# Kernel optimization log

Measured on AMD Instinct MI355X. Metric: run time of the kernel, lower is better.

The kernel has to match this reference:

```python
import jax, jax.numpy as jnp
import numpy as np

TOPK = 2
ROUTE_SCALE = 1.0


def setup_inputs() -> dict:
    key = jax.random.key(0)
    ks = jax.random.split(key, 9)
    B, T, C, E, H = 4, 2048, 1024, 8, 2752
    s = 0.02  # init scale for weights
    return {
        "x": jax.random.normal(ks[0], (B, T, C), dtype=jnp.float32),
        "gate_w": jax.random.normal(ks[1], (E, C), dtype=jnp.float32) * s,
        "expert_bias": jnp.zeros((E,), dtype=jnp.float32),
        "w1": jax.random.normal(ks[2], (E, C, H), dtype=jnp.float32) * s,
        "w2": jax.random.normal(ks[3], (E, H, C), dtype=jnp.float32) * s,
        "w3": jax.random.normal(ks[4], (E, C, H), dtype=jnp.float32) * s,
        "sw1": jax.random.normal(ks[5], (C, H), dtype=jnp.float32) * s,
        "sw2": jax.random.normal(ks[6], (H, C), dtype=jnp.float32) * s,
        "sw3": jax.random.normal(ks[7], (C, H), dtype=jnp.float32) * s,
    }


def reference(x, gate_w, expert_bias, w1, w2, w3, sw1, sw2, sw3):
    B, T, C = x.shape
    E = gate_w.shape[0]
    xf = x.reshape(-1, C)  # (N, C)
    N = xf.shape[0]

    # --- ExpertGate (sigmoid scoring, aux-loss-free, eval mode) ---
    scores = jax.nn.sigmoid(xf @ gate_w.T)            # (N, E), original scores
    routing = scores + expert_bias[None, :]           # bias only affects selection
    _, idx = jax.lax.top_k(routing, TOPK)             # (N, TOPK)
    w = jnp.take_along_axis(scores, idx, axis=1)      # gather original scores
    w = w / (w.sum(axis=-1, keepdims=True) + 1e-8)    # sigmoid normalization
    w = w * ROUTE_SCALE

    # Scatter top-k weights into a dense (N, E) combine matrix
    gates = jnp.zeros((N, E), dtype=xf.dtype)
    gates = gates.at[jnp.arange(N)[:, None], idx].add(w)

    # --- Routed SwiGLU experts (dense compute, gated combine) ---
    y = jnp.zeros_like(xf)
    for e in range(E):  # small fixed loop over experts
        h = jax.nn.silu(xf @ w1[e]) * (xf @ w3[e])    # (N, H)
        y = y + gates[:, e:e + 1] * (h @ w2[e])

    # --- Shared expert (always on) ---
    y = y + (jax.nn.silu(xf @ sw1) * (xf @ sw3)) @ sw2

    return y.reshape(B, T, C)
```

## Files before the change

### kernel.cpp

```cpp
#include <hip/hip_runtime.h>
#include <hip/hip_bf16.h>
#include <stdint.h>

#define E_ 8
#define C_ 1024
#define H_ 2752
#define NTOK 8192
#define CAP_ROWS 17408
#define ROUTED_XB 136
#define SHARED_XB 64
#define SHARED_HBASE 17408
#define HROWS 25600

typedef unsigned short u16;
typedef __attribute__((ext_vector_type(8))) short bf16x8;
typedef __attribute__((ext_vector_type(4))) float f32x4;

static constexpr size_t SZ_XB    = (size_t)NTOK * C_ * 2;
static constexpr size_t SZ_WT    = (size_t)E_ * H_ * C_ * 2;
static constexpr size_t SZ_SWT   = (size_t)H_ * C_ * 2;
static constexpr size_t SZ_H     = (size_t)HROWS * H_ * 2;

static constexpr size_t OFF_XB   = 0;
static constexpr size_t OFF_W1T  = OFF_XB   + SZ_XB;
static constexpr size_t OFF_W3T  = OFF_W1T  + SZ_WT;
static constexpr size_t OFF_W2T  = OFF_W3T  + SZ_WT;
static constexpr size_t OFF_SW1T = OFF_W2T  + SZ_WT;
static constexpr size_t OFF_SW3T = OFF_SW1T + SZ_SWT;
static constexpr size_t OFF_SW2T = OFF_SW3T + SZ_SWT;
static constexpr size_t OFF_H    = OFF_SW2T + SZ_SWT;
static constexpr size_t OFF_RIDX = OFF_H    + SZ_H;
static constexpr size_t OFF_RW   = OFF_RIDX + (size_t)NTOK*2*4;
static constexpr size_t OFF_OFFS = OFF_RW   + (size_t)NTOK*2*4;
static constexpr size_t OFF_PTOK = OFF_OFFS + 64;
static constexpr size_t OFF_PW   = OFF_PTOK + (size_t)CAP_ROWS*4;
static constexpr size_t OFF_INV  = OFF_PW   + (size_t)CAP_ROWS*4;
static constexpr size_t WS_NEED  = OFF_INV  + (size_t)NTOK*2*4;

static constexpr size_t OFF_OUT  = OFF_W1T;

__device__ __forceinline__ u16 f2bf(float f) {
  union { float f; uint32_t u; } v; v.f = f;
  uint32_t r = v.u + 0x7FFFu + ((v.u >> 16) & 1u);
  return (u16)(r >> 16);
}
__device__ __forceinline__ float bfu(uint32_t v) {
  union { uint32_t u; float f; } x; x.u = v << 16; return x.f;
}

__device__ __forceinline__ void gld16(const void* g, void* l) {
  uint32_t lo = (uint32_t)(uintptr_t)l;
  lo = __builtin_amdgcn_readfirstlane(lo);
  __builtin_amdgcn_global_load_lds(
      (const __attribute__((address_space(1))) void*)g,
      (__attribute__((address_space(3))) void*)(uintptr_t)lo, 16, 0, 0);
}

#define MFMA16(A,B,C) __builtin_amdgcn_mfma_f32_16x16x32_bf16((A),(B),(C),0,0,0)

__global__ __launch_bounds__(256) void gate_kernel(
    const float* __restrict__ x, const float* __restrict__ gw,
    const float* __restrict__ bias, u16* __restrict__ xb,
    int* __restrict__ ridx, float* __restrict__ rw)
{
  const int n = blockIdx.x, t = threadIdx.x;
  const float4 v = *(const float4*)(x + (size_t)n * C_ + t * 4);
  union { u16 u[4]; uint2 d; } pk;
  pk.u[0] = f2bf(v.x); pk.u[1] = f2bf(v.y); pk.u[2] = f2bf(v.z); pk.u[3] = f2bf(v.w);
  *(uint2*)(xb + (size_t)n * C_ + t * 4) = pk.d;

  float p[E_];
#pragma unroll
  for (int e = 0; e < E_; ++e) {
    const float4 g = *(const float4*)(gw + (size_t)e * C_ + t * 4);
    p[e] = v.x * g.x + v.y * g.y + v.z * g.z + v.w * g.w;
  }
#pragma unroll
  for (int e = 0; e < E_; ++e)
    for (int off = 32; off > 0; off >>= 1) p[e] += __shfl_down(p[e], off);

  __shared__ float red[4][E_];
  const int wv = t >> 6;
  if ((t & 63) == 0) {
#pragma unroll
    for (int e = 0; e < E_; ++e) red[wv][e] = p[e];
  }
  __syncthreads();
  if (t == 0) {
    float sc[E_], rt[E_];
#pragma unroll
    for (int e = 0; e < E_; ++e) {
      const float d = red[0][e] + red[1][e] + red[2][e] + red[3][e];
      const float s = 1.f / (1.f + expf(-d));
      sc[e] = s; rt[e] = s + bias[e];
    }
    int i0 = 0; float b0 = rt[0];
#pragma unroll
    for (int e = 1; e < E_; ++e) if (rt[e] > b0) { b0 = rt[e]; i0 = e; }
    int i1 = -1; float b1 = -1e30f;
#pragma unroll
    for (int e = 0; e < E_; ++e) if (e != i0 && rt[e] > b1) { b1 = rt[e]; i1 = e; }
    const float s0 = sc[i0], s1 = sc[i1];
    const float inv = 1.f / (s0 + s1 + 1e-8f);
    ridx[2 * n] = i0; ridx[2 * n + 1] = i1;
    rw[2 * n] = s0 * inv; rw[2 * n + 1] = s1 * inv;
  }
}

__global__ __launch_bounds__(256) void transpose_cs_kernel(
    const float* __restrict__ w1, const float* __restrict__ w3,
    const float* __restrict__ sw1, const float* __restrict__ sw3,
    u16* __restrict__ w1t, u16* __restrict__ w3t,
    u16* __restrict__ sw1t, u16* __restrict__ sw3t)
{
  const int z = blockIdx.z;
  const float* src; u16* dst;
  if      (z < 8)  { src = w1 + (size_t)z * C_ * H_;       dst = w1t + (size_t)z * H_ * C_; }
  else if (z < 16) { src = w3 + (size_t)(z - 8) * C_ * H_; dst = w3t + (size_t)(z - 8) * H_ * C_; }
  else if (z == 16){ src = sw1; dst = sw1t; }
  else             { src = sw3; dst = sw3t; }
  __shared__ float tile[32][33];
  const int tx = threadIdx.x, ty = threadIdx.y;
  const int s0 = blockIdx.x * 32;
  const int r0 = blockIdx.y * 32;
#pragma unroll
  for (int i = 0; i < 4; ++i)
    tile[ty + 8 * i][tx] = src[(size_t)(r0 + ty + 8 * i) * H_ + s0 + tx];
  __syncthreads();
#pragma unroll
  for (int i = 0; i < 4; ++i)
    dst[(size_t)(s0 + ty + 8 * i) * C_ + r0 + tx] = f2bf(tile[tx][ty + 8 * i]);
}

__global__ __launch_bounds__(256) void transpose_sc_kernel(
    const float* __restrict__ w2, const float* __restrict__ sw2,
    u16* __restrict__ w2t, u16* __restrict__ sw2t)
{
  const int z = blockIdx.z;
  const float* src; u16* dst;
  if (z < 8) { src = w2 + (size_t)z * H_ * C_; dst = w2t + (size_t)z * C_ * H_; }
  else       { src = sw2; dst = sw2t; }
  __shared__ float tile[32][33];
  const int tx = threadIdx.x, ty = threadIdx.y;
  const int s0 = blockIdx.x * 32;
  const int r0 = blockIdx.y * 32;
#pragma unroll
  for (int i = 0; i < 4; ++i)
    tile[ty + 8 * i][tx] = src[(size_t)(r0 + ty + 8 * i) * C_ + s0 + tx];
  __syncthreads();
#pragma unroll
  for (int i = 0; i < 4; ++i)
    dst[(size_t)(s0 + ty + 8 * i) * H_ + r0 + tx] = f2bf(tile[tx][ty + 8 * i]);
}

__global__ __launch_bounds__(256) void route_scan_kernel(
    const int* __restrict__ ridx, const float* __restrict__ rw,
    int* __restrict__ offsets, int* __restrict__ perm_tok,
    float* __restrict__ perm_w, int* __restrict__ invp)
{
  __shared__ int cnt[256][E_];
  __shared__ int pref[E_][257];
  __shared__ int offs[E_ + 1];
  __shared__ int totals[E_];
  const int t = threadIdx.x;
#pragma unroll
  for (int e = 0; e < E_; ++e) cnt[t][e] = 0;
  for (int j = 0; j < 64; ++j) { const int e = ridx[t * 64 + j]; cnt[t][e]++; }
  __syncthreads();
  if (t < E_) {
    int run = 0;
    for (int i = 0; i < 256; ++i) { pref[t][i] = run; run += cnt[i][t]; }
    totals[t] = run; pref[t][256] = run;
  }
  __syncthreads();
  if (t == 0) {
    int o = 0;
    for (int e = 0; e < E_; ++e) { offs[e] = o; o += (totals[e] + 127) & ~127; }
    offs[E_] = o;
    for (int i = 0; i <= E_; ++i) offsets[i] = offs[i];
  }
  __syncthreads();
#pragma unroll
  for (int e = 0; e < E_; ++e) cnt[t][e] = offs[e] + pref[e][t];
  for (int j = 0; j < 64; ++j) {
    const int a = t * 64 + j;
    const int e = ridx[a];
    const int p = cnt[t][e]++;
    perm_tok[p] = a >> 1;
    perm_w[p] = rw[a];
    invp[a] = p;
  }
  __syncthreads();
  for (int e = 0; e < E_; ++e) {
    for (int p = offs[e] + totals[e] + t; p < offs[e + 1]; p += 256) {
      perm_tok[p] = 0; perm_w[p] = 0.f;
    }
  }
}

__global__ __launch_bounds__(256, 2) void gemm1_m(
    const u16* __restrict__ xb, const u16* __restrict__ w1t_all,
    const u16* __restrict__ w3t_all, const u16* __restrict__ sw1t,
    const u16* __restrict__ sw3t, u16* __restrict__ hbuf,
    const int* __restrict__ offsets, const int* __restrict__ ptok)
{
  __shared__ u16 lds[3 * 8192];
  const int t = threadIdx.x;
  const int n0 = blockIdx.x * 128;
  const int by = blockIdx.y;

  const u16 *b1w, *b3w; int row0; size_t hr0; int gather;
  if (by < ROUTED_XB) {
    row0 = by * 128;
    if (row0 >= offsets[8]) return;
    int e = 0;
#pragma unroll
    for (int i = 0; i < 7; ++i) if (row0 >= offsets[i + 1]) e = i + 1;
    b1w = w1t_all + (size_t)e * (H_ * C_);
    b3w = w3t_all + (size_t)e * (H_ * C_);
    hr0 = (size_t)row0; gather = 1;
  } else {
    row0 = (by - ROUTED_XB) * 128;
    b1w = sw1t; b3w = sw3t; hr0 = (size_t)SHARED_HBASE + row0; gather = 0;
  }

  const int tq = t >> 3;
  const int cb = (((t & 7) ^ (tq & 7)) << 4);
  const char* gA[4]; const char* gB1[4]; const char* gB3[4];
#pragma unroll
  for (int i = 0; i < 4; ++i) {
    const int m = i * 32 + tq;
    const int tok = gather ? ptok[row0 + m] : (row0 + m);
    gA[i] = (const char*)xb + (size_t)tok * (C_ * 2) + cb;
    int nn = n0 + m; if (nn > H_ - 1) nn = H_ - 1;
    gB1[i] = (const char*)b1w + (size_t)nn * (C_ * 2) + cb;
    gB3[i] = (const char*)b3w + (size_t)nn * (C_ * 2) + cb;
  }
  char* lwave = (char*)lds + (t >> 6) * 1024;

  f32x4 acc1[4][4], acc3[4][4];
#pragma unroll
  for (int i = 0; i < 4; ++i)
#pragma unroll
    for (int j = 0; j < 4; ++j) { acc1[i][j] = f32x4{0,0,0,0}; acc3[i][j] = f32x4{0,0,0,0}; }

  const int lane = t & 63;
  const int l15 = lane & 15, lhi = lane >> 4, swz = lane & 7;
  const int wm = (t >> 7) & 1, wn = (t >> 6) & 1;
  int arow[4], brow[4];
#pragma unroll
  for (int f = 0; f < 4; ++f) {
    arow[f] = (wm * 64 + f * 16 + l15) * 128;
    brow[f] = (wn * 64 + f * 16 + l15) * 128;
  }
  const char* ldsc = (const char*)lds;

  for (int kt = 0; kt < C_ / 64; ++kt) {
    const int kb = kt * 128;
#pragma unroll
    for (int i = 0; i < 4; ++i) gld16(gA[i]  + kb, lwave + i * 4096);
#pragma unroll
    for (int i = 0; i < 4; ++i) gld16(gB1[i] + kb, lwave + 16384 + i * 4096);
#pragma unroll
    for (int i = 0; i < 4; ++i) gld16(gB3[i] + kb, lwave + 32768 + i * 4096);
    __syncthreads();
#pragma unroll
    for (int kk = 0; kk < 2; ++kk) {
      const int co = ((((kk << 2) | lhi)) ^ swz) << 4;
      bf16x8 a[4], b1[4], b3[4];
#pragma unroll
      for (int f = 0; f < 4; ++f) a[f]  = *(const bf16x8*)(ldsc + arow[f] + co);
#pragma unroll
      for (int f = 0; f < 4; ++f) b1[f] = *(const bf16x8*)(ldsc + 16384 + brow[f] + co);
#pragma unroll
      for (int f = 0; f < 4; ++f) b3[f] = *(const bf16x8*)(ldsc + 32768 + brow[f] + co);
#pragma unroll
      for (int mf = 0; mf < 4; ++mf)
#pragma unroll
        for (int nf = 0; nf < 4; ++nf) {
          acc1[mf][nf] = MFMA16(a[mf], b1[nf], acc1[mf][nf]);
          acc3[mf][nf] = MFMA16(a[mf], b3[nf], acc3[mf][nf]);
        }
    }
    __syncthreads();
  }

  const int rbase = wm * 64 + lhi * 4;
  const int cbase = n0 + wn * 64 + l15;
#pragma unroll
  for (int mf = 0; mf < 4; ++mf)
#pragma unroll
    for (int q = 0; q < 4; ++q) {
      const int r = rbase + mf * 16 + q;
      u16* hrow = hbuf + (hr0 + r) * H_;
#pragma unroll
      for (int nf = 0; nf < 4; ++nf) {
        const int c = cbase + nf * 16;
        if (c < H_) {
          const float v1 = acc1[mf][nf][q], v3 = acc3[mf][nf][q];
          const float sv = v1 / (1.f + __expf(-v1));
          hrow[c] = f2bf(sv * v3);
        }
      }
    }
}

__global__ __launch_bounds__(256, 2) void gemm2_m(
    const u16* __restrict__ hbuf, const u16* __restrict__ w2t_all,
    const u16* __restrict__ sw2t, u16* __restrict__ outb,
    const int* __restrict__ offsets)
{
  __shared__ u16 lds[2 * 8192];
  const int t = threadIdx.x;
  const int n0 = blockIdx.x * 128;
  const int by = blockIdx.y;

  int row0; size_t hr0; const u16* bW;
  if (by < ROUTED_XB) {
    row0 = by * 128;
    if (row0 >= offsets[8]) return;
    int e = 0;
#pragma unroll
    for (int i = 0; i < 7; ++i) if (row0 >= offsets[i + 1]) e = i + 1;
    bW = w2t_all + (size_t)e * (C_ * H_);
    hr0 = (size_t)row0;
  } else {
    row0 = (by - ROUTED_XB) * 128;
    bW = sw2t; hr0 = (size_t)SHARED_HBASE + row0;
  }

  const int tq = t >> 3;
  const int cb = (((t & 7) ^ (tq & 7)) << 4);
  const char* gA[4]; const char* gB[4];
#pragma unroll
  for (int i = 0; i < 4; ++i) {
    const int m = i * 32 + tq;
    gA[i] = (const char*)hbuf + (hr0 + m) * (size_t)(H_ * 2) + cb;
    gB[i] = (const char*)bW + (size_t)(n0 + m) * (H_ * 2) + cb;
  }
  char* lwave = (char*)lds + (t >> 6) * 1024;

  f32x4 acc[4][4];
#pragma unroll
  for (int i = 0; i < 4; ++i)
#pragma unroll
    for (int j = 0; j < 4; ++j) acc[i][j] = f32x4{0,0,0,0};

  const int lane = t & 63;
  const int l15 = lane & 15, lhi = lane >> 4, swz = lane & 7;
  const int wm = (t >> 7) & 1, wn = (t >> 6) & 1;
  int arow[4], brow[4];
#pragma unroll
  for (int f = 0; f < 4; ++f) {
    arow[f] = (wm * 64 + f * 16 + l15) * 128;
    brow[f] = (wn * 64 + f * 16 + l15) * 128;
  }
  const char* ldsc = (const char*)lds;

  for (int kt = 0; kt < 43; ++kt) {
    const int kb = kt * 128;
#pragma unroll
    for (int i = 0; i < 4; ++i) gld16(gA[i] + kb, lwave + i * 4096);
#pragma unroll
    for (int i = 0; i < 4; ++i) gld16(gB[i] + kb, lwave + 16384 + i * 4096);
    __syncthreads();
#pragma unroll
    for (int kk = 0; kk < 2; ++kk) {
      const int co = ((((kk << 2) | lhi)) ^ swz) << 4;
      bf16x8 a[4], b[4];
#pragma unroll
      for (int f = 0; f < 4; ++f) a[f] = *(const bf16x8*)(ldsc + arow[f] + co);
#pragma unroll
      for (int f = 0; f < 4; ++f) b[f] = *(const bf16x8*)(ldsc + 16384 + brow[f] + co);
#pragma unroll
      for (int mf = 0; mf < 4; ++mf)
#pragma unroll
        for (int nf = 0; nf < 4; ++nf)
          acc[mf][nf] = MFMA16(a[mf], b[nf], acc[mf][nf]);
    }
    __syncthreads();
  }

  const int rbase = wm * 64 + lhi * 4;
  const int cbase = n0 + wn * 64 + l15;
#pragma unroll
  for (int mf = 0; mf < 4; ++mf)
#pragma unroll
    for (int q = 0; q < 4; ++q) {
      u16* orow = outb + (hr0 + rbase + mf * 16 + q) * C_;
#pragma unroll
      for (int nf = 0; nf < 4; ++nf)
        orow[cbase + nf * 16] = f2bf(acc[mf][nf][q]);
    }
}

__global__ __launch_bounds__(256) void combine_kernel(
    const u16* __restrict__ outb, const int* __restrict__ invp,
    const float* __restrict__ rw, float* __restrict__ y)
{
  const int n = blockIdx.x, t = threadIdx.x;
  const int c4 = t * 4;
  const int p0 = invp[2 * n], p1 = invp[2 * n + 1];
  const float g0 = rw[2 * n], g1 = rw[2 * n + 1];
  const uint2 s = *(const uint2*)(outb + ((size_t)SHARED_HBASE + n) * C_ + c4);
  const uint2 a = *(const uint2*)(outb + (size_t)p0 * C_ + c4);
  const uint2 b = *(const uint2*)(outb + (size_t)p1 * C_ + c4);
  float4 o;
  o.x = bfu(s.x & 0xffffu) + g0 * bfu(a.x & 0xffffu) + g1 * bfu(b.x & 0xffffu);
  o.y = bfu(s.x >> 16)     + g0 * bfu(a.x >> 16)     + g1 * bfu(b.x >> 16);
  o.z = bfu(s.y & 0xffffu) + g0 * bfu(a.y & 0xffffu) + g1 * bfu(b.y & 0xffffu);
  o.w = bfu(s.y >> 16)     + g0 * bfu(a.y >> 16)     + g1 * bfu(b.y >> 16);
  *(float4*)(y + (size_t)n * C_ + c4) = o;
}

extern "C" void kernel_launch(void* const* d_in, const int* in_sizes, int n_in,
                              void* d_out, int out_size, void* d_ws, size_t ws_size,
                              hipStream_t stream)
{
  const float* x    = (const float*)d_in[0];
  const float* gw   = (const float*)d_in[1];
  const float* bias = (const float*)d_in[2];
  const float* w1   = (const float*)d_in[3];
  const float* w2   = (const float*)d_in[4];
  const float* w3   = (const float*)d_in[5];
  const float* sw1  = (const float*)d_in[6];
  const float* sw2  = (const float*)d_in[7];
  const float* sw3  = (const float*)d_in[8];
  float* y = (float*)d_out;
  char* ws = (char*)d_ws;
  if (ws_size < WS_NEED) return;

  u16*   xb    = (u16*)(ws + OFF_XB);
  u16*   w1t   = (u16*)(ws + OFF_W1T);
  u16*   w3t   = (u16*)(ws + OFF_W3T);
  u16*   w2t   = (u16*)(ws + OFF_W2T);
  u16*   sw1t  = (u16*)(ws + OFF_SW1T);
  u16*   sw3t  = (u16*)(ws + OFF_SW3T);
  u16*   sw2t  = (u16*)(ws + OFF_SW2T);
  u16*   hbuf  = (u16*)(ws + OFF_H);
  u16*   outb  = (u16*)(ws + OFF_OUT);
  int*   ridx  = (int*)(ws + OFF_RIDX);
  float* rwt   = (float*)(ws + OFF_RW);
  int*   offs  = (int*)(ws + OFF_OFFS);
  int*   ptok  = (int*)(ws + OFF_PTOK);
  float* pw    = (float*)(ws + OFF_PW);
  int*   invp  = (int*)(ws + OFF_INV);

  gate_kernel<<<NTOK, 256, 0, stream>>>(x, gw, bias, xb, ridx, rwt);
  transpose_cs_kernel<<<dim3(H_ / 32, C_ / 32, 18), dim3(32, 8), 0, stream>>>(
      w1, w3, sw1, sw3, w1t, w3t, sw1t, sw3t);
  transpose_sc_kernel<<<dim3(C_ / 32, H_ / 32, 9), dim3(32, 8), 0, stream>>>(
      w2, sw2, w2t, sw2t);
  route_scan_kernel<<<1, 256, 0, stream>>>(ridx, rwt, offs, ptok, pw, invp);

  gemm1_m<<<dim3(22, ROUTED_XB + SHARED_XB), 256, 0, stream>>>(
      xb, w1t, w3t, sw1t, sw3t, hbuf, offs, ptok);
  gemm2_m<<<dim3(8, ROUTED_XB + SHARED_XB), 256, 0, stream>>>(
      hbuf, w2t, sw2t, outb, offs);
  combine_kernel<<<NTOK, 256, 0, stream>>>(outb, invp, rwt, y);
}
```

Before: 667.1 us.

## Double gemm2 K-tile to 256 and widen weight-transpose tiles to 64 rows

The down-projection GEMM now stages 256-wide K slices in LDS instead of 128-wide ones. It uses a 16-way XOR swizzle and a peeled tail step for the leftover 128 K elements, which halves the number of load/barrier rounds per output tile. Both weight transpose kernels now process 64x32 tiles with a flat 256-thread block, so each stored output row segment is 64 bf16 values wide and writes coalesce better. The cost is double the LDS per gemm2 block, which can limit occupancy. The tail stage also reads 128 bytes past the end of each K row, though those values are never used.

```diff
diff --git a/kernel.cpp b/kernel.cpp
--- a/kernel.cpp
+++ b/kernel.cpp
@@ -119,17 +119,21 @@
   else if (z < 16) { src = w3 + (size_t)(z - 8) * C_ * H_; dst = w3t + (size_t)(z - 8) * H_ * C_; }
   else if (z == 16){ src = sw1; dst = sw1t; }
   else             { src = sw3; dst = sw3t; }
-  __shared__ float tile[32][33];
-  const int tx = threadIdx.x, ty = threadIdx.y;
+  __shared__ float tile[64][33];
+  const int t = threadIdx.x;
   const int s0 = blockIdx.x * 32;
-  const int r0 = blockIdx.y * 32;
-#pragma unroll
-  for (int i = 0; i < 4; ++i)
+  const int r0 = blockIdx.y * 64;
+  const int tx = t & 31, ty = t >> 5;
+#pragma unroll
+  for (int i = 0; i < 8; ++i)
     tile[ty + 8 * i][tx] = src[(size_t)(r0 + ty + 8 * i) * H_ + s0 + tx];
   __syncthreads();
-#pragma unroll
-  for (int i = 0; i < 4; ++i)
-    dst[(size_t)(s0 + ty + 8 * i) * C_ + r0 + tx] = f2bf(tile[tx][ty + 8 * i]);
+  const int tx2 = t & 63, ty2 = t >> 6;
+#pragma unroll
+  for (int i = 0; i < 8; ++i) {
+    const int hh = ty2 + 4 * i;
+    dst[(size_t)(s0 + hh) * C_ + r0 + tx2] = f2bf(tile[tx2][hh]);
+  }
 }
 
 __global__ __launch_bounds__(256) void transpose_sc_kernel(
@@ -140,17 +144,21 @@
   const float* src; u16* dst;
   if (z < 8) { src = w2 + (size_t)z * H_ * C_; dst = w2t + (size_t)z * C_ * H_; }
   else       { src = sw2; dst = sw2t; }
-  __shared__ float tile[32][33];
-  const int tx = threadIdx.x, ty = threadIdx.y;
+  __shared__ float tile[64][33];
+  const int t = threadIdx.x;
   const int s0 = blockIdx.x * 32;
-  const int r0 = blockIdx.y * 32;
-#pragma unroll
-  for (int i = 0; i < 4; ++i)
+  const int r0 = blockIdx.y * 64;
+  const int tx = t & 31, ty = t >> 5;
+#pragma unroll
+  for (int i = 0; i < 8; ++i)
     tile[ty + 8 * i][tx] = src[(size_t)(r0 + ty + 8 * i) * C_ + s0 + tx];
   __syncthreads();
-#pragma unroll
-  for (int i = 0; i < 4; ++i)
-    dst[(size_t)(s0 + ty + 8 * i) * H_ + r0 + tx] = f2bf(tile[tx][ty + 8 * i]);
+  const int tx2 = t & 63, ty2 = t >> 6;
+#pragma unroll
+  for (int i = 0; i < 8; ++i) {
+    const int cc = ty2 + 4 * i;
+    dst[(size_t)(s0 + cc) * H_ + r0 + tx2] = f2bf(tile[tx2][cc]);
+  }
 }
 
 __global__ __launch_bounds__(256) void route_scan_kernel(
@@ -310,7 +318,7 @@
     const u16* __restrict__ sw2t, u16* __restrict__ outb,
     const int* __restrict__ offsets)
 {
-  __shared__ u16 lds[2 * 8192];
+  __shared__ u16 lds[2 * 16384];
   const int t = threadIdx.x;
   const int n0 = blockIdx.x * 128;
   const int by = blockIdx.y;
@@ -329,12 +337,12 @@
     bW = sw2t; hr0 = (size_t)SHARED_HBASE + row0;
   }
 
-  const int tq = t >> 3;
-  const int cb = (((t & 7) ^ (tq & 7)) << 4);
-  const char* gA[4]; const char* gB[4];
-#pragma unroll
-  for (int i = 0; i < 4; ++i) {
-    const int m = i * 32 + tq;
+  const int tq = t >> 4;
+  const int cb = (((t & 15) ^ (tq & 15)) << 4);
+  const char* gA[8]; const char* gB[8];
+#pragma unroll
+  for (int i = 0; i < 8; ++i) {
+    const int m = i * 16 + tq;
     gA[i] = (const char*)hbuf + (hr0 + m) * (size_t)(H_ * 2) + cb;
     gB[i] = (const char*)bW + (size_t)(n0 + m) * (H_ * 2) + cb;
   }
@@ -347,39 +355,41 @@
     for (int j = 0; j < 4; ++j) acc[i][j] = f32x4{0,0,0,0};
 
   const int lane = t & 63;
-  const int l15 = lane & 15, lhi = lane >> 4, swz = lane & 7;
+  const int l15 = lane & 15, lhi = lane >> 4;
   const int wm = (t >> 7) & 1, wn = (t >> 6) & 1;
   int arow[4], brow[4];
 #pragma unroll
   for (int f = 0; f < 4; ++f) {
-    arow[f] = (wm * 64 + f * 16 + l15) * 128;
-    brow[f] = (wn * 64 + f * 16 + l15) * 128;
+    arow[f] = (wm * 64 + f * 16 + l15) * 256;
+    brow[f] = (wn * 64 + f * 16 + l15) * 256;
   }
   const char* ldsc = (const char*)lds;
 
-  for (int kt = 0; kt < 43; ++kt) {
-    const int kb = kt * 128;
-#pragma unroll
-    for (int i = 0; i < 4; ++i) gld16(gA[i] + kb, lwave + i * 4096);
-#pragma unroll
-    for (int i = 0; i < 4; ++i) gld16(gB[i] + kb, lwave + 16384 + i * 4096);
+#define G2_STAGE(kb) do { \
+  _Pragma("unroll") for (int i = 0; i < 8; ++i) gld16(gA[i] + (kb), lwave + i * 4096); \
+  _Pragma("unroll") for (int i = 0; i < 8; ++i) gld16(gB[i] + (kb), lwave + 32768 + i * 4096); } while (0)
+#define G2_KK(kk) do { \
+  const int co = ((((kk) << 2) | lhi) ^ l15) << 4; \
+  bf16x8 a[4], b[4]; \
+  _Pragma("unroll") for (int f = 0; f < 4; ++f) a[f] = *(const bf16x8*)(ldsc + arow[f] + co); \
+  _Pragma("unroll") for (int f = 0; f < 4; ++f) b[f] = *(const bf16x8*)(ldsc + 32768 + brow[f] + co); \
+  _Pragma("unroll") for (int mf = 0; mf < 4; ++mf) \
+    _Pragma("unroll") for (int nf = 0; nf < 4; ++nf) \
+      acc[mf][nf] = MFMA16(a[mf], b[nf], acc[mf][nf]); } while (0)
+
+  for (int kt = 0; kt < 21; ++kt) {
+    G2_STAGE(kt * 256);
     __syncthreads();
 #pragma unroll
-    for (int kk = 0; kk < 2; ++kk) {
-      const int co = ((((kk << 2) | lhi)) ^ swz) << 4;
-      bf16x8 a[4], b[4];
-#pragma unroll
-      for (int f = 0; f < 4; ++f) a[f] = *(const bf16x8*)(ldsc + arow[f] + co);
-#pragma unroll
-      for (int f = 0; f < 4; ++f) b[f] = *(const bf16x8*)(ldsc + 16384 + brow[f] + co);
-#pragma unroll
-      for (int mf = 0; mf < 4; ++mf)
-#pragma unroll
-        for (int nf = 0; nf < 4; ++nf)
-          acc[mf][nf] = MFMA16(a[mf], b[nf], acc[mf][nf]);
-    }
+    for (int kk = 0; kk < 4; ++kk) G2_KK(kk);
     __syncthreads();
   }
+  G2_STAGE(21 * 256);
+  __syncthreads();
+  G2_KK(0); G2_KK(1);
+
+#undef G2_STAGE
+#undef G2_KK
 
   const int rbase = wm * 64 + lhi * 4;
   const int cbase = n0 + wn * 64 + l15;
@@ -447,9 +457,9 @@
   int*   invp  = (int*)(ws + OFF_INV);
 
   gate_kernel<<<NTOK, 256, 0, stream>>>(x, gw, bias, xb, ridx, rwt);
-  transpose_cs_kernel<<<dim3(H_ / 32, C_ / 32, 18), dim3(32, 8), 0, stream>>>(
+  transpose_cs_kernel<<<dim3(H_ / 32, C_ / 64, 18), 256, 0, stream>>>(
       w1, w3, sw1, sw3, w1t, w3t, sw1t, sw3t);
-  transpose_sc_kernel<<<dim3(C_ / 32, H_ / 32, 9), dim3(32, 8), 0, stream>>>(
+  transpose_sc_kernel<<<dim3(C_ / 32, H_ / 64, 9), 256, 0, stream>>>(
       w2, sw2, w2t, sw2t);
   route_scan_kernel<<<1, 256, 0, stream>>>(ridx, rwt, offs, ptok, pw, invp);
 
```

Result: no change. 668.5 us (+0.2%).

## Widen gemm2 N-tile to 256 and use 64x32 transpose tiles

Applied to the files above, without the earlier changes.

The down-projection GEMM now computes a 128x256 output tile per block. Each wave holds 4x8 MFMA accumulators and the LDS buffer grows to fit the wider B tile, which cuts the number of times each block of A rows is reloaded across N. The weight transpose kernels move to 256-thread 1D blocks with 64-row tiles, so each bf16 write row is 64 elements wide instead of 32. The costs are higher register and LDS use per block, which may cut occupancy or cause spills, and only 4 column blocks for gemm2.

```diff
diff --git a/kernel.cpp b/kernel.cpp
--- a/kernel.cpp
+++ b/kernel.cpp
@@ -119,17 +119,21 @@
   else if (z < 16) { src = w3 + (size_t)(z - 8) * C_ * H_; dst = w3t + (size_t)(z - 8) * H_ * C_; }
   else if (z == 16){ src = sw1; dst = sw1t; }
   else             { src = sw3; dst = sw3t; }
-  __shared__ float tile[32][33];
-  const int tx = threadIdx.x, ty = threadIdx.y;
+  __shared__ float tile[64][33];
+  const int t = threadIdx.x;
   const int s0 = blockIdx.x * 32;
-  const int r0 = blockIdx.y * 32;
-#pragma unroll
-  for (int i = 0; i < 4; ++i)
+  const int r0 = blockIdx.y * 64;
+  const int tx = t & 31, ty = t >> 5;
+#pragma unroll
+  for (int i = 0; i < 8; ++i)
     tile[ty + 8 * i][tx] = src[(size_t)(r0 + ty + 8 * i) * H_ + s0 + tx];
   __syncthreads();
-#pragma unroll
-  for (int i = 0; i < 4; ++i)
-    dst[(size_t)(s0 + ty + 8 * i) * C_ + r0 + tx] = f2bf(tile[tx][ty + 8 * i]);
+  const int tx2 = t & 63, ty2 = t >> 6;
+#pragma unroll
+  for (int i = 0; i < 8; ++i) {
+    const int hh = ty2 + 4 * i;
+    dst[(size_t)(s0 + hh) * C_ + r0 + tx2] = f2bf(tile[tx2][hh]);
+  }
 }
 
 __global__ __launch_bounds__(256) void transpose_sc_kernel(
@@ -140,17 +144,21 @@
   const float* src; u16* dst;
   if (z < 8) { src = w2 + (size_t)z * H_ * C_; dst = w2t + (size_t)z * C_ * H_; }
   else       { src = sw2; dst = sw2t; }
-  __shared__ float tile[32][33];
-  const int tx = threadIdx.x, ty = threadIdx.y;
+  __shared__ float tile[64][33];
+  const int t = threadIdx.x;
   const int s0 = blockIdx.x * 32;
-  const int r0 = blockIdx.y * 32;
-#pragma unroll
-  for (int i = 0; i < 4; ++i)
+  const int r0 = blockIdx.y * 64;
+  const int tx = t & 31, ty = t >> 5;
+#pragma unroll
+  for (int i = 0; i < 8; ++i)
     tile[ty + 8 * i][tx] = src[(size_t)(r0 + ty + 8 * i) * C_ + s0 + tx];
   __syncthreads();
-#pragma unroll
-  for (int i = 0; i < 4; ++i)
-    dst[(size_t)(s0 + ty + 8 * i) * H_ + r0 + tx] = f2bf(tile[tx][ty + 8 * i]);
+  const int tx2 = t & 63, ty2 = t >> 6;
+#pragma unroll
+  for (int i = 0; i < 8; ++i) {
+    const int cc = ty2 + 4 * i;
+    dst[(size_t)(s0 + cc) * H_ + r0 + tx2] = f2bf(tile[tx2][cc]);
+  }
 }
 
 __global__ __launch_bounds__(256) void route_scan_kernel(
@@ -310,9 +318,9 @@
     const u16* __restrict__ sw2t, u16* __restrict__ outb,
     const int* __restrict__ offsets)
 {
-  __shared__ u16 lds[2 * 8192];
+  __shared__ u16 lds[3 * 8192];
   const int t = threadIdx.x;
-  const int n0 = blockIdx.x * 128;
+  const int n0 = blockIdx.x * 256;
   const int by = blockIdx.y;
 
   int row0; size_t hr0; const u16* bW;
@@ -331,30 +339,29 @@
 
   const int tq = t >> 3;
   const int cb = (((t & 7) ^ (tq & 7)) << 4);
-  const char* gA[4]; const char* gB[4];
-#pragma unroll
-  for (int i = 0; i < 4; ++i) {
-    const int m = i * 32 + tq;
-    gA[i] = (const char*)hbuf + (hr0 + m) * (size_t)(H_ * 2) + cb;
-    gB[i] = (const char*)bW + (size_t)(n0 + m) * (H_ * 2) + cb;
-  }
+  const char* gA[4]; const char* gB[8];
+#pragma unroll
+  for (int i = 0; i < 4; ++i)
+    gA[i] = (const char*)hbuf + (hr0 + i * 32 + tq) * (size_t)(H_ * 2) + cb;
+#pragma unroll
+  for (int i = 0; i < 8; ++i)
+    gB[i] = (const char*)bW + (size_t)(n0 + i * 32 + tq) * (H_ * 2) + cb;
   char* lwave = (char*)lds + (t >> 6) * 1024;
 
-  f32x4 acc[4][4];
+  f32x4 acc[4][8];
 #pragma unroll
   for (int i = 0; i < 4; ++i)
 #pragma unroll
-    for (int j = 0; j < 4; ++j) acc[i][j] = f32x4{0,0,0,0};
+    for (int j = 0; j < 8; ++j) acc[i][j] = f32x4{0,0,0,0};
 
   const int lane = t & 63;
   const int l15 = lane & 15, lhi = lane >> 4, swz = lane & 7;
-  const int wm = (t >> 7) & 1, wn = (t >> 6) & 1;
-  int arow[4], brow[4];
-#pragma unroll
-  for (int f = 0; f < 4; ++f) {
-    arow[f] = (wm * 64 + f * 16 + l15) * 128;
-    brow[f] = (wn * 64 + f * 16 + l15) * 128;
-  }
+  const int wv = t >> 6, wm = wv >> 1, wn = wv & 1;
+  int arow[4], brow[8];
+#pragma unroll
+  for (int f = 0; f < 4; ++f) arow[f] = (wm * 64 + f * 16 + l15) * 128;
+#pragma unroll
+  for (int f = 0; f < 8; ++f) brow[f] = (wn * 128 + f * 16 + l15) * 128;
   const char* ldsc = (const char*)lds;
 
   for (int kt = 0; kt < 43; ++kt) {
@@ -362,34 +369,34 @@
 #pragma unroll
     for (int i = 0; i < 4; ++i) gld16(gA[i] + kb, lwave + i * 4096);
 #pragma unroll
-    for (int i = 0; i < 4; ++i) gld16(gB[i] + kb, lwave + 16384 + i * 4096);
+    for (int i = 0; i < 8; ++i) gld16(gB[i] + kb, lwave + 16384 + i * 4096);
     __syncthreads();
 #pragma unroll
     for (int kk = 0; kk < 2; ++kk) {
       const int co = ((((kk << 2) | lhi)) ^ swz) << 4;
-      bf16x8 a[4], b[4];
+      bf16x8 a[4], b[8];
 #pragma unroll
       for (int f = 0; f < 4; ++f) a[f] = *(const bf16x8*)(ldsc + arow[f] + co);
 #pragma unroll
-      for (int f = 0; f < 4; ++f) b[f] = *(const bf16x8*)(ldsc + 16384 + brow[f] + co);
+      for (int f = 0; f < 8; ++f) b[f] = *(const bf16x8*)(ldsc + 16384 + brow[f] + co);
 #pragma unroll
       for (int mf = 0; mf < 4; ++mf)
 #pragma unroll
-        for (int nf = 0; nf < 4; ++nf)
+        for (int nf = 0; nf < 8; ++nf)
           acc[mf][nf] = MFMA16(a[mf], b[nf], acc[mf][nf]);
     }
     __syncthreads();
   }
 
   const int rbase = wm * 64 + lhi * 4;
-  const int cbase = n0 + wn * 64 + l15;
+  const int cbase = n0 + wn * 128 + l15;
 #pragma unroll
   for (int mf = 0; mf < 4; ++mf)
 #pragma unroll
     for (int q = 0; q < 4; ++q) {
       u16* orow = outb + (hr0 + rbase + mf * 16 + q) * C_;
 #pragma unroll
-      for (int nf = 0; nf < 4; ++nf)
+      for (int nf = 0; nf < 8; ++nf)
         orow[cbase + nf * 16] = f2bf(acc[mf][nf][q]);
     }
 }
@@ -447,15 +454,15 @@
   int*   invp  = (int*)(ws + OFF_INV);
 
   gate_kernel<<<NTOK, 256, 0, stream>>>(x, gw, bias, xb, ridx, rwt);
-  transpose_cs_kernel<<<dim3(H_ / 32, C_ / 32, 18), dim3(32, 8), 0, stream>>>(
+  transpose_cs_kernel<<<dim3(H_ / 32, C_ / 64, 18), 256, 0, stream>>>(
       w1, w3, sw1, sw3, w1t, w3t, sw1t, sw3t);
-  transpose_sc_kernel<<<dim3(C_ / 32, H_ / 32, 9), dim3(32, 8), 0, stream>>>(
+  transpose_sc_kernel<<<dim3(C_ / 32, H_ / 64, 9), 256, 0, stream>>>(
       w2, sw2, w2t, sw2t);
   route_scan_kernel<<<1, 256, 0, stream>>>(ridx, rwt, offs, ptok, pw, invp);
 
   gemm1_m<<<dim3(22, ROUTED_XB + SHARED_XB), 256, 0, stream>>>(
       xb, w1t, w3t, sw1t, sw3t, hbuf, offs, ptok);
-  gemm2_m<<<dim3(8, ROUTED_XB + SHARED_XB), 256, 0, stream>>>(
+  gemm2_m<<<dim3(4, ROUTED_XB + SHARED_XB), 256, 0, stream>>>(
       hbuf, w2t, sw2t, outb, offs);
   combine_kernel<<<NTOK, 256, 0, stream>>>(outb, invp, rwt, y);
 }
```

After: 637.8 us. -4.4%, faster.
